# Kernel optimization log

Hardware: AMD Instinct MI355X
Metric: run time of the kernel (lower is better)

Reference implementation:

```python
import jax, jax.numpy as jnp
import numpy as np

N, K, B, D, T = 30000, 32, 8, 256, 10
NC = T + 1            # int_small_classes
LB_COL, UB_COL = 21, 22
INF = 1e18


def _ln(x, g, b, eps=1e-5):
    m = jnp.mean(x, axis=-1, keepdims=True)
    v = jnp.mean((x - m) ** 2, axis=-1, keepdims=True)
    return (x - m) * jax.lax.rsqrt(v + eps) * g + b


def _head(x, ng, nb, W1, b1, W2, b2, Wh, bh):
    # LayerNorm -> Linear -> GELU -> Linear -> GELU -> residual -> head (dropout off: eval)
    h = _ln(x, ng, nb)
    h = jax.nn.gelu(h @ W1.T + b1, approximate=False)
    h = jax.nn.gelu(h @ W2.T + b2, approximate=False)
    return (x + h) @ Wh.T + bh


def setup_inputs():
    key = jax.random.key(0)
    ks = jax.random.split(key, 32)
    s = 0.05
    inp = {}
    inp['evolved_tokens'] = jax.random.normal(ks[0], (B * K, D), jnp.float32)
    inp['var_batch'] = jnp.sort(jax.random.randint(ks[1], (N,), 0, B))
    aw = jax.random.uniform(ks[2], (N, K), jnp.float32)
    inp['attn_weights'] = aw / aw.sum(-1, keepdims=True)
    inp['var_types'] = jax.random.randint(ks[3], (N,), 0, 3)
    inp['z_var_0'] = jax.random.normal(ks[4], (N, D), jnp.float32)
    vf = 0.1 * jax.random.normal(ks[5], (N, 23), jnp.float32)
    lb = jnp.floor(jax.random.uniform(ks[6], (N,), minval=-5.0, maxval=0.0))
    ub = lb + jnp.floor(jax.random.uniform(ks[7], (N,), minval=0.0, maxval=30.0))
    ub = jnp.where(jax.random.uniform(ks[8], (N,)) < 0.1, 1e19, ub)
    inp['variable_features'] = vf.at[:, LB_COL].set(lb).at[:, UB_COL].set(ub)
    # deslice proj + fusion norm
    inp['Wp'] = s * jax.random.normal(ks[9], (D, D), jnp.float32)
    inp['bp'] = jnp.zeros((D,), jnp.float32)
    inp['fn_g'] = jnp.ones((D,), jnp.float32)
    inp['fn_b'] = jnp.zeros((D,), jnp.float32)
    # three decoder heads
    i = 10
    for name, out in (('bin', 1), ('ints', NC), ('intl', 1)):
        inp[name + '_ng'] = jnp.ones((D,), jnp.float32)
        inp[name + '_nb'] = jnp.zeros((D,), jnp.float32)
        inp[name + '_W1'] = s * jax.random.normal(ks[i], (D, D), jnp.float32)
        inp[name + '_b1'] = jnp.zeros((D,), jnp.float32)
        inp[name + '_W2'] = s * jax.random.normal(ks[i + 1], (D, D), jnp.float32)
        inp[name + '_b2'] = jnp.zeros((D,), jnp.float32)
        inp[name + '_Wh'] = s * jax.random.normal(ks[i + 2], (out, D), jnp.float32)
        inp[name + '_bh'] = (jnp.full((out,), -0.5, jnp.float32) if name == 'bin'
                             else jnp.zeros((out,), jnp.float32))
        i += 3
    return inp


def reference(evolved_tokens, var_batch, attn_weights, var_types, z_var_0,
              variable_features, Wp, bp, fn_g, fn_b,
              bin_ng, bin_nb, bin_W1, bin_b1, bin_W2, bin_b2, bin_Wh, bin_bh,
              ints_ng, ints_nb, ints_W1, ints_b1, ints_W2, ints_b2, ints_Wh, ints_bh,
              intl_ng, intl_nb, intl_W1, intl_b1, intl_W2, intl_b2, intl_Wh, intl_bh):
    # 1. deslice: attn_weights @ projected evolved tokens of the variable's graph
    proj = evolved_tokens @ Wp.T + bp          # [B*K, D]
    tok3 = proj.reshape(B, K, D)
    z_des = jnp.einsum('nk,nkd->nd', attn_weights, tok3[var_batch])  # [N, D]
    # 2. residual fusion + LayerNorm
    z_out = _ln(z_des + z_var_0, fn_g, fn_b)
    # 3. routing (extract_int_routing)
    lb = variable_features[:, LB_COL]
    ub = variable_features[:, UB_COL]
    is_int = var_types == 2
    finite = (jnp.abs(lb) < INF) & (jnp.abs(ub) < INF)
    mask_int_small = is_int & finite & ((ub - lb) <= T)
    mask_int_large = is_int & ~mask_int_small
    mask_bin = var_types == 1
    offsets = jnp.floor(lb)                                   # [N]
    ranges = jnp.clip(jnp.ceil(ub) - offsets + 1.0, 1.0, NC).astype(jnp.int32)  # [N]
    # 4. decode. Heads are evaluated densely on all N rows; the original's
    #    gather->MLP->scatter equals row-selection of these dense outputs.
    prob_bin = jax.nn.sigmoid(_head(z_out, bin_ng, bin_nb, bin_W1, bin_b1,
                                    bin_W2, bin_b2, bin_Wh, bin_bh))   # [N, 1]
    logits = _head(z_out, ints_ng, ints_nb, ints_W1, ints_b1,
                   ints_W2, ints_b2, ints_Wh, ints_bh)                 # [N, NC]
    valid = jnp.arange(NC)[None, :] < ranges[:, None]
    logits = jnp.where(valid, logits, -1e9)  # dynamic logit masking of invalid classes
    pred_large = _head(z_out, intl_ng, intl_nb, intl_W1, intl_b1,
                       intl_W2, intl_b2, intl_Wh, intl_bh)             # [N, 1]
    return (z_out, prob_bin, logits, pred_large,
            mask_bin, mask_int_small, mask_int_large, offsets, ranges)
```

## Files before the change

### kernel.cpp

```cpp
#include <hip/hip_runtime.h>
#include <math.h>

#define NV   30000
#define DD   256
#define KK   32
#define NCLS 11
#define NT   469

#define OZ  0
#define OPB 7680000
#define OLG 7710000
#define OPL 8040000
#define OMB 8070000
#define OMS 8100000
#define OML 8130000
#define OOF 8160000
#define ORG 8190000

typedef __bf16 bf16x8 __attribute__((ext_vector_type(8)));
typedef float  f32x4  __attribute__((ext_vector_type(4)));

__device__ __forceinline__ unsigned short f2b(float f) {
    unsigned u = __float_as_uint(f);
    u += 0x7fffu + ((u >> 16) & 1u);
    return (unsigned short)(u >> 16);
}

__device__ __forceinline__ float gelu_f(float x) {
    float x2 = x * x;
    float m = x * __builtin_fmaf(-0.0713548163f, x2, -1.5957691216f);
    float e = __expf(m);
    return x * __builtin_amdgcn_rcpf(1.0f + e);
}

__device__ __forceinline__ int swz(int row) { return (row + (row >> 3)) & 7; }
__device__ __forceinline__ int lidx(int row, int col) {
    return row * 256 + ((((col) >> 3) ^ swz(row)) << 3) + (col & 7);
}
__device__ __forceinline__ int physchunk(int ck, int row) {
    return (ck & ~7) | ((ck & 7) ^ swz(row));
}

struct WP {
    const float *W1, *ng, *nb, *b1, *W2, *Wh;
    unsigned short *W1e, *W2b, *Whb;
    float *b1e, *swh;
    int nc;
};

__global__ void k_prep(const float* __restrict__ et, const float* __restrict__ Wp,
                       const float* __restrict__ bp, unsigned short* __restrict__ projT,
                       const float* __restrict__ vf, const int* __restrict__ vt,
                       float* __restrict__ out,
                       WP wa, WP wb, WP wc) {
    __shared__ float es[DD];
    __shared__ float red[4], red2[4];
    if (blockIdx.y == 0) {
        int r = blockIdx.x, c = threadIdx.x;
        es[c] = et[r * DD + c];
        __syncthreads();
        const float4* w4 = (const float4*)(Wp + c * DD);
        float a0 = 0.f, a1 = 0.f, a2 = 0.f, a3 = 0.f;
#pragma unroll 16
        for (int d = 0; d < DD / 4; ++d) {
            float4 w = w4[d];
            a0 += es[4 * d] * w.x;
            a1 += es[4 * d + 1] * w.y;
            a2 += es[4 * d + 2] * w.z;
            a3 += es[4 * d + 3] * w.w;
        }
        float acc = bp[c] + ((a0 + a1) + (a2 + a3));
        projT[c * DD + r] = f2b(acc);
        return;
    }
    if (blockIdx.y == 4) {
        int n = blockIdx.x * 256 + threadIdx.x;
        if (n < NV) {
            float lb = vf[n * 23 + 21], ub = vf[n * 23 + 22];
            int t = vt[n];
            bool is_int = (t == 2);
            bool finite = (fabsf(lb) < 1e18f) && (fabsf(ub) < 1e18f);
            bool small_ = is_int && finite && (ub - lb <= 10.0f);
            float off = floorf(lb);
            float rngf = ceilf(ub) - off + 1.0f;
            rngf = fminf(fmaxf(rngf, 1.0f), (float)NCLS);
            out[OMB + n] = (t == 1) ? 1.0f : 0.0f;
            out[OMS + n] = small_ ? 1.0f : 0.0f;
            out[OML + n] = (is_int && !small_) ? 1.0f : 0.0f;
            out[OOF + n] = off;
            out[ORG + n] = (float)((int)rngf);
        }
        return;
    }
    WP wp = (blockIdx.y == 1) ? wa : ((blockIdx.y == 2) ? wb : wc);
    int j = blockIdx.x, d = threadIdx.x;
    float v1 = wp.W1[j * DD + d];
    wp.W1e[j * DD + d] = f2b(v1 * wp.ng[d]);
    wp.W2b[j * DD + d] = f2b(wp.W2[j * DD + d]);
    float p2 = 0.f;
    if (j < 16) {
        p2 = (j < wp.nc) ? wp.Wh[j * DD + d] : 0.f;
        wp.Whb[j * DD + d] = f2b(p2);
    }
    float p = v1 * wp.nb[d];
#pragma unroll
    for (int m = 1; m < 64; m <<= 1) { p += __shfl_xor(p, m); p2 += __shfl_xor(p2, m); }
    if ((d & 63) == 0) { red[d >> 6] = p; red2[d >> 6] = p2; }
    __syncthreads();
    if (d == 0) {
        wp.b1e[j] = wp.b1[j] + red[0] + red[1] + red[2] + red[3];
        if (j < 16) wp.swh[j] = red2[0] + red2[1] + red2[2] + red2[3];
    }
}

__global__ __launch_bounds__(512)
void k_zout(const unsigned short* __restrict__ projT, const int* __restrict__ vb,
            const float* __restrict__ aw, const float* __restrict__ z0,
            const float* __restrict__ g, const float* __restrict__ b,
            const unsigned short* __restrict__ Whb, const float* __restrict__ swh,
            float* __restrict__ out, unsigned short* __restrict__ zhat,
            float* __restrict__ zwhT) {
    __shared__ unsigned short Al[64 * 256];
    __shared__ float sqs[64 * 8], sqq[64 * 8];
    __shared__ float mvm[64], mvr[64], sig[64];
    __shared__ float gs[DD], bs[DD];
    __shared__ float swhs[48];
    int tid = threadIdx.x;
    int lane = tid & 63, wv = tid >> 6;
    int l15 = lane & 15, lq = lane >> 4;
    int n0 = blockIdx.x * 64;

    int bmin = vb[n0];
    int bmax = vb[(n0 + 63 < NV) ? (n0 + 63) : (NV - 1)];

    if (tid < 256) gs[tid] = g[tid];
    else           bs[tid - 256] = b[tid - 256];
    if (tid < 48) swhs[tid] = swh[tid];
    {
        uint4 z4 = make_uint4(0, 0, 0, 0);
        uint4* dst = (uint4*)Al;
#pragma unroll
        for (int j = 0; j < 4; ++j) dst[tid + j * 512] = z4;
    }
    __syncthreads();
    {
        int r = tid >> 3, sub = tid & 7;
        int n = n0 + r;
        if (n < NV) {
            int bb = vb[n];
            float4 a4 = *(const float4*)(aw + (size_t)n * KK + sub * 4);
            int j0 = bb * 32 + sub * 4;
            int phys = r * 256 + (physchunk(j0 >> 3, r) << 3) + (j0 & 7);
            ushort4 u;
            u.x = f2b(a4.x); u.y = f2b(a4.y); u.z = f2b(a4.z); u.w = f2b(a4.w);
            *(ushort4*)(Al + phys) = u;
        }
    }
    __syncthreads();

    int nb0 = wv * 32;
    f32x4 acc[4][2];
#pragma unroll
    for (int mt = 0; mt < 4; ++mt)
#pragma unroll
        for (int nt = 0; nt < 2; ++nt) acc[mt][nt] = f32x4{0.f, 0.f, 0.f, 0.f};

    {
        const unsigned short* Bb = projT + (size_t)(nb0 + l15) * DD + lq * 8;
        for (int ks = bmin; ks <= bmax; ++ks) {
            bf16x8 bfr[2];
#pragma unroll
            for (int nt = 0; nt < 2; ++nt)
                bfr[nt] = *(const bf16x8*)(Bb + nt * 16 * DD + ks * 32);
            int ck = ks * 4 + lq;
#pragma unroll
            for (int mt = 0; mt < 4; ++mt) {
                int row = mt * 16 + l15;
                bf16x8 afr = *(const bf16x8*)(Al + row * 256 + (physchunk(ck, row) << 3));
#pragma unroll
                for (int nt = 0; nt < 2; ++nt)
                    acc[mt][nt] = __builtin_amdgcn_mfma_f32_16x16x32_bf16(afr, bfr[nt], acc[mt][nt], 0, 0, 0);
            }
        }
    }
#pragma unroll
    for (int mt = 0; mt < 4; ++mt)
#pragma unroll
        for (int nt = 0; nt < 2; ++nt) {
            int col = nb0 + nt * 16 + l15;
#pragma unroll
            for (int r = 0; r < 4; ++r) {
                int n = n0 + mt * 16 + lq * 4 + r;
                float zv = (n < NV) ? z0[(size_t)n * DD + col] : 0.f;
                acc[mt][nt][r] += zv;
            }
        }
#pragma unroll
    for (int mt = 0; mt < 4; ++mt)
#pragma unroll
        for (int r = 0; r < 4; ++r) {
            float s = acc[mt][0][r] + acc[mt][1][r];
            float q = acc[mt][0][r] * acc[mt][0][r] + acc[mt][1][r] * acc[mt][1][r];
#pragma unroll
            for (int m = 1; m < 16; m <<= 1) { s += __shfl_xor(s, m); q += __shfl_xor(q, m); }
            if (l15 == 0) { int row = mt * 16 + lq * 4 + r; sqs[row * 8 + wv] = s; sqq[row * 8 + wv] = q; }
        }
    __syncthreads();
    if (tid < 64) {
        float s = 0.f, q = 0.f;
#pragma unroll
        for (int w = 0; w < 8; ++w) { s += sqs[tid * 8 + w]; q += sqq[tid * 8 + w]; }
        float mean = s * (1.f / DD);
        float var  = q * (1.f / DD) - mean * mean;
        mvm[tid] = mean; mvr[tid] = rsqrtf(var + 1e-5f);
    }
    __syncthreads();
    float zb[4][2][4];
#pragma unroll
    for (int mt = 0; mt < 4; ++mt)
#pragma unroll
        for (int nt = 0; nt < 2; ++nt) {
            int col = nb0 + nt * 16 + l15;
#pragma unroll
            for (int r = 0; r < 4; ++r) {
                int row = mt * 16 + lq * 4 + r;
                float z = (acc[mt][nt][r] - mvm[row]) * mvr[row] * gs[col] + bs[col];
                zb[mt][nt][r] = z;
                int n = n0 + row;
                if (n < NV) out[OZ + (size_t)n * DD + col] = z;
            }
        }
#pragma unroll
    for (int mt = 0; mt < 4; ++mt)
#pragma unroll
        for (int r = 0; r < 4; ++r) {
            float s = zb[mt][0][r] + zb[mt][1][r];
            float q = zb[mt][0][r] * zb[mt][0][r] + zb[mt][1][r] * zb[mt][1][r];
#pragma unroll
            for (int m = 1; m < 16; m <<= 1) { s += __shfl_xor(s, m); q += __shfl_xor(q, m); }
            if (l15 == 0) { int row = mt * 16 + lq * 4 + r; sqs[row * 8 + wv] = s; sqq[row * 8 + wv] = q; }
        }
    __syncthreads();
    if (tid < 64) {
        float s = 0.f, q = 0.f;
#pragma unroll
        for (int w = 0; w < 8; ++w) { s += sqs[tid * 8 + w]; q += sqq[tid * 8 + w]; }
        float m2 = s * (1.f / DD);
        float v2 = q * (1.f / DD) - m2 * m2;
        float r2 = rsqrtf(v2 + 1e-5f);
        mvm[tid] = m2; mvr[tid] = r2; sig[tid] = (v2 + 1e-5f) * r2;
    }
    __syncthreads();
#pragma unroll
    for (int mt = 0; mt < 4; ++mt)
#pragma unroll
        for (int nt = 0; nt < 2; ++nt) {
            int col = nb0 + nt * 16 + l15;
#pragma unroll
            for (int r = 0; r < 4; ++r) {
                int row = mt * 16 + lq * 4 + r;
                Al[lidx(row, col)] = f2b((zb[mt][nt][r] - mvm[row]) * mvr[row]);
            }
        }
    __syncthreads();
    if (wv < 4) {
        f32x4 ac2[3];
#pragma unroll
        for (int mf = 0; mf < 3; ++mf) ac2[mf] = f32x4{0.f, 0.f, 0.f, 0.f};
        const unsigned short* Ab = Whb + (size_t)l15 * DD + lq * 8;
        int rowb = wv * 16 + l15;
#pragma unroll
        for (int ks = 0; ks < 8; ++ks) {
            int ck = ks * 4 + lq;
            bf16x8 bb2 = *(const bf16x8*)(Al + rowb * 256 + (physchunk(ck, rowb) << 3));
#pragma unroll
            for (int mf = 0; mf < 3; ++mf) {
                bf16x8 aa2 = *(const bf16x8*)(Ab + (size_t)mf * 16 * DD + ks * 32);
                ac2[mf] = __builtin_amdgcn_mfma_f32_16x16x32_bf16(aa2, bb2, ac2[mf], 0, 0, 0);
            }
        }
        int nl = wv * 16 + l15;
        float sg = sig[nl], mu = mvm[nl];
#pragma unroll
        for (int mf = 0; mf < 3; ++mf)
#pragma unroll
            for (int r = 0; r < 4; ++r) {
                int o = mf * 16 + lq * 4 + r;
                zwhT[(size_t)blockIdx.x * 3072 + o * 64 + nl] = sg * ac2[mf][r] + mu * swhs[o];
            }
    }
    {
        uint4* dstg = (uint4*)(zhat + (size_t)n0 * 256);
        const uint4* srcl = (const uint4*)Al;
#pragma unroll
        for (int j = 0; j < 4; ++j) dstg[tid + j * 512] = srcl[tid + j * 512];
    }
}

struct HeadP {
    const unsigned short *W1e, *W2b, *Whb;
    const float *b1e, *b2, *bh;
    int nc;
};

__global__ __launch_bounds__(512, 4)
void k_heads(const unsigned short* __restrict__ zhat, const float* __restrict__ zwhT,
             const float* __restrict__ ranges,
             HeadP h0, HeadP h1p, HeadP h2p,
             float* __restrict__ opb, float* __restrict__ olg, float* __restrict__ opl) {
    __shared__ unsigned short hl1[64 * 256];
    __shared__ unsigned short hl2[64 * 256];
    __shared__ float b1s[DD], b2s[DD];
    __shared__ float zws[16 * 64];
    __shared__ float rgs[64];
    __shared__ float bhs[16];

    int head = blockIdx.x / NT;
    int tile = blockIdx.x % NT;
    HeadP hp = (head == 0) ? h0 : ((head == 1) ? h1p : h2p);
    int nc = hp.nc;
    int n0 = tile * 64;
    int tid = threadIdx.x, lane = tid & 63, wv = tid >> 6;
    int l15 = lane & 15, lq = lane >> 4;
    int M0 = wv * 32;

    {
        const uint4* src = (const uint4*)(zhat + (size_t)n0 * 256);
        uint4* dst = (uint4*)hl1;
#pragma unroll
        for (int j = 0; j < 4; ++j) dst[tid + j * 512] = src[tid + j * 512];
    }
    if (tid < 256) b1s[tid] = hp.b1e[tid];
    else           b2s[tid - 256] = hp.b2[tid - 256];
    ((float2*)zws)[tid] = ((const float2*)(zwhT + (size_t)(tile * 3 + head) * 1024))[tid];
    if (tid < 64) { int n = n0 + tid; rgs[tid] = (n < NV) ? ranges[n] : 0.f; }
    else if (tid < 80) { int o = tid - 64; bhs[o] = (o < nc) ? hp.bh[o] : 0.f; }
    __syncthreads();

    const unsigned short* Ab1 = hp.W1e + (size_t)(M0 + l15) * DD + lq * 8;
    const unsigned short* Ab2 = hp.W2b + (size_t)(M0 + l15) * DD + lq * 8;

    f32x4 acc[2][4];
#pragma unroll
    for (int mt = 0; mt < 2; ++mt)
#pragma unroll
        for (int nt = 0; nt < 4; ++nt) acc[mt][nt] = f32x4{0.f, 0.f, 0.f, 0.f};

    bf16x8 afr[3][2];
#pragma unroll
    for (int mt = 0; mt < 2; ++mt) {
        afr[0][mt] = *(const bf16x8*)(Ab1 + mt * 16 * DD);
        afr[1][mt] = *(const bf16x8*)(Ab1 + mt * 16 * DD + 32);
    }

#pragma unroll
    for (int ks = 0; ks < 8; ++ks) {
        int cur = ks % 3;
        if (ks < 6) {
#pragma unroll
            for (int mt = 0; mt < 2; ++mt)
                afr[(ks + 2) % 3][mt] = *(const bf16x8*)(Ab1 + mt * 16 * DD + (ks + 2) * 32);
        }
        int ck = ks * 4 + lq;
        bf16x8 bfr[4];
#pragma unroll
        for (int nt = 0; nt < 4; ++nt) {
            int row = nt * 16 + l15;
            bfr[nt] = *(const bf16x8*)(hl1 + row * 256 + (physchunk(ck, row) << 3));
        }
#pragma unroll
        for (int nt = 0; nt < 4; ++nt)
#pragma unroll
            for (int mt = 0; mt < 2; ++mt)
                acc[mt][nt] = __builtin_amdgcn_mfma_f32_16x16x32_bf16(afr[cur][mt], bfr[nt], acc[mt][nt], 0, 0, 0);
    }

#pragma unroll
    for (int mt = 0; mt < 2; ++mt) {
        afr[0][mt] = *(const bf16x8*)(Ab2 + mt * 16 * DD);
        afr[1][mt] = *(const bf16x8*)(Ab2 + mt * 16 * DD + 32);
    }

#pragma unroll
    for (int mt = 0; mt < 2; ++mt) {
        int jb = M0 + mt * 16 + lq * 4;
        float4 bias = *(const float4*)(b1s + jb);
        int chunk = jb >> 3;
#pragma unroll
        for (int nt = 0; nt < 4; ++nt) {
            int n = nt * 16 + l15;
            ushort4 u;
            u.x = f2b(gelu_f(acc[mt][nt][0] + bias.x));
            u.y = f2b(gelu_f(acc[mt][nt][1] + bias.y));
            u.z = f2b(gelu_f(acc[mt][nt][2] + bias.z));
            u.w = f2b(gelu_f(acc[mt][nt][3] + bias.w));
            *(ushort4*)(hl2 + n * 256 + (physchunk(chunk, n) << 3) + (jb & 7)) = u;
        }
    }
    __syncthreads();

#pragma unroll
    for (int mt = 0; mt < 2; ++mt)
#pragma unroll
        for (int nt = 0; nt < 4; ++nt) acc[mt][nt] = f32x4{0.f, 0.f, 0.f, 0.f};
#pragma unroll
    for (int ks = 0; ks < 8; ++ks) {
        int cur = ks % 3;
        if (ks < 6) {
#pragma unroll
            for (int mt = 0; mt < 2; ++mt)
                afr[(ks + 2) % 3][mt] = *(const bf16x8*)(Ab2 + mt * 16 * DD + (ks + 2) * 32);
        }
        int ck = ks * 4 + lq;
        bf16x8 bfr[4];
#pragma unroll
        for (int nt = 0; nt < 4; ++nt) {
            int row = nt * 16 + l15;
            bfr[nt] = *(const bf16x8*)(hl2 + row * 256 + (physchunk(ck, row) << 3));
        }
#pragma unroll
        for (int nt = 0; nt < 4; ++nt)
#pragma unroll
            for (int mt = 0; mt < 2; ++mt)
                acc[mt][nt] = __builtin_amdgcn_mfma_f32_16x16x32_bf16(afr[cur][mt], bfr[nt], acc[mt][nt], 0, 0, 0);
    }

    bf16x8 apr = *(const bf16x8*)(hp.Whb + (size_t)l15 * DD + wv * 32 + lq * 8);

#pragma unroll
    for (int mt = 0; mt < 2; ++mt) {
        int jb = M0 + mt * 16 + lq * 4;
        float4 bias = *(const float4*)(b2s + jb);
        int chunk = jb >> 3;
#pragma unroll
        for (int nt = 0; nt < 4; ++nt) {
            int n = nt * 16 + l15;
            ushort4 u;
            u.x = f2b(gelu_f(acc[mt][nt][0] + bias.x));
            u.y = f2b(gelu_f(acc[mt][nt][1] + bias.y));
            u.z = f2b(gelu_f(acc[mt][nt][2] + bias.z));
            u.w = f2b(gelu_f(acc[mt][nt][3] + bias.w));
            *(ushort4*)(hl1 + n * 256 + (physchunk(chunk, n) << 3) + (jb & 7)) = u;
        }
    }
    __syncthreads();

    f32x4 ap[4];
#pragma unroll
    for (int nt = 0; nt < 4; ++nt) ap[nt] = f32x4{0.f, 0.f, 0.f, 0.f};
    {
        int ck = wv * 4 + lq;
#pragma unroll
        for (int nt = 0; nt < 4; ++nt) {
            int row = nt * 16 + l15;
            bf16x8 bfr = *(const bf16x8*)(hl1 + row * 256 + (physchunk(ck, row) << 3));
            ap[nt] = __builtin_amdgcn_mfma_f32_16x16x32_bf16(apr, bfr, ap[nt], 0, 0, 0);
        }
    }
    {
        float* pb = (float*)hl2;
#pragma unroll
        for (int nt = 0; nt < 4; ++nt)
#pragma unroll
            for (int r = 0; r < 4; ++r)
                pb[wv * 1024 + (lq * 4 + r) * 64 + nt * 16 + l15] = ap[nt][r];
    }
    __syncthreads();

    const float* pb = (const float*)hl2;
    for (int idx = tid; idx < 64 * nc; idx += 512) {
        int o = idx >> 6, n = idx & 63;
        float val = bhs[o] + zws[o * 64 + n];
#pragma unroll
        for (int w = 0; w < 8; ++w) val += pb[w * 1024 + o * 64 + n];
        int ng = n0 + n;
        if (ng < NV) {
            if (head == 0)      opb[ng] = __builtin_amdgcn_rcpf(1.f + __expf(-val));
            else if (head == 2) opl[ng] = val;
            else {
                int rng = (int)rgs[n];
                olg[(size_t)ng * NCLS + o] = (o < rng) ? val : -1e9f;
            }
        }
    }
}

extern "C" void kernel_launch(void* const* d_in, const int* in_sizes, int n_in,
                              void* d_out, int out_size, void* d_ws, size_t ws_size,
                              hipStream_t stream) {
    const float* et = (const float*)d_in[0];
    const int*   vb = (const int*)d_in[1];
    const float* aw = (const float*)d_in[2];
    const int*   vt = (const int*)d_in[3];
    const float* z0 = (const float*)d_in[4];
    const float* vf = (const float*)d_in[5];
    const float* Wp = (const float*)d_in[6];
    const float* bp = (const float*)d_in[7];
    const float* fg = (const float*)d_in[8];
    const float* fb = (const float*)d_in[9];
    float* out = (float*)d_out;

    char* ws = (char*)d_ws;
    unsigned short* projT = (unsigned short*)ws;
    float* b1e           = (float*)(ws + 131072);
    unsigned short* W1e  = (unsigned short*)(ws + 134144);
    unsigned short* W2b  = (unsigned short*)(ws + 527360);
    unsigned short* Whb  = (unsigned short*)(ws + 920576);
    float* swh           = (float*)(ws + 945152);
    float* zwhT          = (float*)(ws + 945408);
    unsigned short* zhat = (unsigned short*)(ws + 6708480);

    WP wps[3];
    for (int h = 0; h < 3; ++h) {
        wps[h].W1 = (const float*)d_in[12 + 8 * h];
        wps[h].ng = (const float*)d_in[10 + 8 * h];
        wps[h].nb = (const float*)d_in[11 + 8 * h];
        wps[h].b1 = (const float*)d_in[13 + 8 * h];
        wps[h].W2 = (const float*)d_in[14 + 8 * h];
        wps[h].Wh = (const float*)d_in[16 + 8 * h];
        wps[h].W1e = W1e + h * 65536;
        wps[h].W2b = W2b + h * 65536;
        wps[h].Whb = Whb + h * 4096;
        wps[h].b1e = b1e + h * 256;
        wps[h].swh = swh + h * 16;
        wps[h].nc  = (h == 1) ? NCLS : 1;
    }
    k_prep<<<dim3(256, 5), 256, 0, stream>>>(et, Wp, bp, projT, vf, vt, out,
                                             wps[0], wps[1], wps[2]);

    k_zout<<<NT, 512, 0, stream>>>(projT, vb, aw, z0, fg, fb, Whb, swh,
                                   out, zhat, zwhT);

    HeadP hps[3];
    for (int h = 0; h < 3; ++h) {
        hps[h].W1e = W1e + h * 65536;
        hps[h].W2b = W2b + h * 65536;
        hps[h].Whb = Whb + h * 4096;
        hps[h].b1e = b1e + h * 256;
        hps[h].b2  = (const float*)d_in[15 + 8 * h];
        hps[h].bh  = (const float*)d_in[17 + 8 * h];
        hps[h].nc  = (h == 1) ? NCLS : 1;
    }
    k_heads<<<3 * NT, 512, 0, stream>>>(zhat, zwhT, out + ORG,
                                        hps[0], hps[1], hps[2],
                                        out + OPB, out + OLG, out + OPL);
}
```

Measured before the change: 235.6 us.

## Fuse z_out computation and three decoder heads into a single kernel

Merges the z_out/LayerNorm kernel with the per-head MLP kernel. Each 64-row block now keeps the normalized tile in LDS and loops over the three heads itself, so the bf16 zhat and zwhT round-trips through global memory go away, along with one launch. The final head projection is also reworked as a direct MFMA on four waves instead of an 8-way partial-sum reduction. In exchange, the grid drops from 3*NT blocks to NT blocks, and each block runs the three heads serially, which cuts parallelism across the GPU.

```diff
diff --git a/kernel.cpp b/kernel.cpp
--- a/kernel.cpp
+++ b/kernel.cpp
@@ -113,22 +113,37 @@
     }
 }
 
-__global__ __launch_bounds__(512)
-void k_zout(const unsigned short* __restrict__ projT, const int* __restrict__ vb,
+struct HeadP {
+    const unsigned short *W1e, *W2b, *Whb;
+    const float *b1e, *b2, *bh;
+    int nc;
+};
+
+__global__ __launch_bounds__(512, 4)
+void k_main(const unsigned short* __restrict__ projT, const int* __restrict__ vb,
             const float* __restrict__ aw, const float* __restrict__ z0,
             const float* __restrict__ g, const float* __restrict__ b,
             const unsigned short* __restrict__ Whb, const float* __restrict__ swh,
-            float* __restrict__ out, unsigned short* __restrict__ zhat,
-            float* __restrict__ zwhT) {
+            const float* __restrict__ ranges,
+            HeadP h0, HeadP h1p, HeadP h2p,
+            float* __restrict__ out, float* __restrict__ opb,
+            float* __restrict__ olg, float* __restrict__ opl) {
     __shared__ unsigned short Al[64 * 256];
-    __shared__ float sqs[64 * 8], sqq[64 * 8];
+    __shared__ unsigned short hl2[64 * 256];
+    __shared__ float b1s[DD], b2s[DD];
+    __shared__ float zws[48 * 64];
     __shared__ float mvm[64], mvr[64], sig[64];
-    __shared__ float gs[DD], bs[DD];
     __shared__ float swhs[48];
+
     int tid = threadIdx.x;
     int lane = tid & 63, wv = tid >> 6;
     int l15 = lane & 15, lq = lane >> 4;
     int n0 = blockIdx.x * 64;
+
+    float* gs = zws;
+    float* bs = zws + 256;
+    float* sqs = (float*)hl2;
+    float* sqq = (float*)hl2 + 512;
 
     int bmin = vb[n0];
     int bmax = vb[(n0 + 63 < NV) ? (n0 + 63) : (NV - 1)];
@@ -164,7 +179,6 @@
     for (int mt = 0; mt < 4; ++mt)
 #pragma unroll
         for (int nt = 0; nt < 2; ++nt) acc[mt][nt] = f32x4{0.f, 0.f, 0.f, 0.f};
-
     {
         const unsigned short* Bb = projT + (size_t)(nb0 + l15) * DD + lq * 8;
         for (int ks = bmin; ks <= bmax; ++ks) {
@@ -215,7 +229,6 @@
         mvm[tid] = mean; mvr[tid] = rsqrtf(var + 1e-5f);
     }
     __syncthreads();
-    float zb[4][2][4];
 #pragma unroll
     for (int mt = 0; mt < 4; ++mt)
 #pragma unroll
@@ -225,7 +238,7 @@
             for (int r = 0; r < 4; ++r) {
                 int row = mt * 16 + lq * 4 + r;
                 float z = (acc[mt][nt][r] - mvm[row]) * mvr[row] * gs[col] + bs[col];
-                zb[mt][nt][r] = z;
+                acc[mt][nt][r] = z;
                 int n = n0 + row;
                 if (n < NV) out[OZ + (size_t)n * DD + col] = z;
             }
@@ -234,8 +247,8 @@
     for (int mt = 0; mt < 4; ++mt)
 #pragma unroll
         for (int r = 0; r < 4; ++r) {
-            float s = zb[mt][0][r] + zb[mt][1][r];
-            float q = zb[mt][0][r] * zb[mt][0][r] + zb[mt][1][r] * zb[mt][1][r];
+            float s = acc[mt][0][r] + acc[mt][1][r];
+            float q = acc[mt][0][r] * acc[mt][0][r] + acc[mt][1][r] * acc[mt][1][r];
 #pragma unroll
             for (int m = 1; m < 16; m <<= 1) { s += __shfl_xor(s, m); q += __shfl_xor(q, m); }
             if (l15 == 0) { int row = mt * 16 + lq * 4 + r; sqs[row * 8 + wv] = s; sqq[row * 8 + wv] = q; }
@@ -259,7 +272,7 @@
 #pragma unroll
             for (int r = 0; r < 4; ++r) {
                 int row = mt * 16 + lq * 4 + r;
-                Al[lidx(row, col)] = f2b((zb[mt][nt][r] - mvm[row]) * mvr[row]);
+                Al[lidx(row, col)] = f2b((acc[mt][nt][r] - mvm[row]) * mvr[row]);
             }
         }
     __syncthreads();
@@ -286,200 +299,152 @@
 #pragma unroll
             for (int r = 0; r < 4; ++r) {
                 int o = mf * 16 + lq * 4 + r;
-                zwhT[(size_t)blockIdx.x * 3072 + o * 64 + nl] = sg * ac2[mf][r] + mu * swhs[o];
-            }
-    }
-    {
-        uint4* dstg = (uint4*)(zhat + (size_t)n0 * 256);
-        const uint4* srcl = (const uint4*)Al;
-#pragma unroll
-        for (int j = 0; j < 4; ++j) dstg[tid + j * 512] = srcl[tid + j * 512];
-    }
-}
-
-struct HeadP {
-    const unsigned short *W1e, *W2b, *Whb;
-    const float *b1e, *b2, *bh;
-    int nc;
-};
-
-__global__ __launch_bounds__(512, 4)
-void k_heads(const unsigned short* __restrict__ zhat, const float* __restrict__ zwhT,
-             const float* __restrict__ ranges,
-             HeadP h0, HeadP h1p, HeadP h2p,
-             float* __restrict__ opb, float* __restrict__ olg, float* __restrict__ opl) {
-    __shared__ unsigned short hl1[64 * 256];
-    __shared__ unsigned short hl2[64 * 256];
-    __shared__ float b1s[DD], b2s[DD];
-    __shared__ float zws[16 * 64];
-    __shared__ float rgs[64];
-    __shared__ float bhs[16];
-
-    int head = blockIdx.x / NT;
-    int tile = blockIdx.x % NT;
-    HeadP hp = (head == 0) ? h0 : ((head == 1) ? h1p : h2p);
-    int nc = hp.nc;
-    int n0 = tile * 64;
-    int tid = threadIdx.x, lane = tid & 63, wv = tid >> 6;
-    int l15 = lane & 15, lq = lane >> 4;
-    int M0 = wv * 32;
-
-    {
-        const uint4* src = (const uint4*)(zhat + (size_t)n0 * 256);
-        uint4* dst = (uint4*)hl1;
-#pragma unroll
-        for (int j = 0; j < 4; ++j) dst[tid + j * 512] = src[tid + j * 512];
-    }
-    if (tid < 256) b1s[tid] = hp.b1e[tid];
-    else           b2s[tid - 256] = hp.b2[tid - 256];
-    ((float2*)zws)[tid] = ((const float2*)(zwhT + (size_t)(tile * 3 + head) * 1024))[tid];
-    if (tid < 64) { int n = n0 + tid; rgs[tid] = (n < NV) ? ranges[n] : 0.f; }
-    else if (tid < 80) { int o = tid - 64; bhs[o] = (o < nc) ? hp.bh[o] : 0.f; }
-    __syncthreads();
-
-    const unsigned short* Ab1 = hp.W1e + (size_t)(M0 + l15) * DD + lq * 8;
-    const unsigned short* Ab2 = hp.W2b + (size_t)(M0 + l15) * DD + lq * 8;
-
-    f32x4 acc[2][4];
-#pragma unroll
-    for (int mt = 0; mt < 2; ++mt)
-#pragma unroll
-        for (int nt = 0; nt < 4; ++nt) acc[mt][nt] = f32x4{0.f, 0.f, 0.f, 0.f};
-
-    bf16x8 afr[3][2];
-#pragma unroll
-    for (int mt = 0; mt < 2; ++mt) {
-        afr[0][mt] = *(const bf16x8*)(Ab1 + mt * 16 * DD);
-        afr[1][mt] = *(const bf16x8*)(Ab1 + mt * 16 * DD + 32);
-    }
-
-#pragma unroll
-    for (int ks = 0; ks < 8; ++ks) {
-        int cur = ks % 3;
-        if (ks < 6) {
-#pragma unroll
-            for (int mt = 0; mt < 2; ++mt)
-                afr[(ks + 2) % 3][mt] = *(const bf16x8*)(Ab1 + mt * 16 * DD + (ks + 2) * 32);
-        }
-        int ck = ks * 4 + lq;
-        bf16x8 bfr[4];
-#pragma unroll
-        for (int nt = 0; nt < 4; ++nt) {
-            int row = nt * 16 + l15;
-            bfr[nt] = *(const bf16x8*)(hl1 + row * 256 + (physchunk(ck, row) << 3));
-        }
-#pragma unroll
-        for (int nt = 0; nt < 4; ++nt)
-#pragma unroll
-            for (int mt = 0; mt < 2; ++mt)
-                acc[mt][nt] = __builtin_amdgcn_mfma_f32_16x16x32_bf16(afr[cur][mt], bfr[nt], acc[mt][nt], 0, 0, 0);
-    }
-
-#pragma unroll
-    for (int mt = 0; mt < 2; ++mt) {
-        afr[0][mt] = *(const bf16x8*)(Ab2 + mt * 16 * DD);
-        afr[1][mt] = *(const bf16x8*)(Ab2 + mt * 16 * DD + 32);
-    }
-
-#pragma unroll
-    for (int mt = 0; mt < 2; ++mt) {
-        int jb = M0 + mt * 16 + lq * 4;
-        float4 bias = *(const float4*)(b1s + jb);
-        int chunk = jb >> 3;
-#pragma unroll
-        for (int nt = 0; nt < 4; ++nt) {
-            int n = nt * 16 + l15;
-            ushort4 u;
-            u.x = f2b(gelu_f(acc[mt][nt][0] + bias.x));
-            u.y = f2b(gelu_f(acc[mt][nt][1] + bias.y));
-            u.z = f2b(gelu_f(acc[mt][nt][2] + bias.z));
-            u.w = f2b(gelu_f(acc[mt][nt][3] + bias.w));
-            *(ushort4*)(hl2 + n * 256 + (physchunk(chunk, n) << 3) + (jb & 7)) = u;
-        }
-    }
-    __syncthreads();
-
-#pragma unroll
-    for (int mt = 0; mt < 2; ++mt)
-#pragma unroll
-        for (int nt = 0; nt < 4; ++nt) acc[mt][nt] = f32x4{0.f, 0.f, 0.f, 0.f};
-#pragma unroll
-    for (int ks = 0; ks < 8; ++ks) {
-        int cur = ks % 3;
-        if (ks < 6) {
-#pragma unroll
-            for (int mt = 0; mt < 2; ++mt)
-                afr[(ks + 2) % 3][mt] = *(const bf16x8*)(Ab2 + mt * 16 * DD + (ks + 2) * 32);
-        }
-        int ck = ks * 4 + lq;
-        bf16x8 bfr[4];
-#pragma unroll
-        for (int nt = 0; nt < 4; ++nt) {
-            int row = nt * 16 + l15;
-            bfr[nt] = *(const bf16x8*)(hl2 + row * 256 + (physchunk(ck, row) << 3));
-        }
-#pragma unroll
-        for (int nt = 0; nt < 4; ++nt)
-#pragma unroll
-            for (int mt = 0; mt < 2; ++mt)
-                acc[mt][nt] = __builtin_amdgcn_mfma_f32_16x16x32_bf16(afr[cur][mt], bfr[nt], acc[mt][nt], 0, 0, 0);
-    }
-
-    bf16x8 apr = *(const bf16x8*)(hp.Whb + (size_t)l15 * DD + wv * 32 + lq * 8);
-
-#pragma unroll
-    for (int mt = 0; mt < 2; ++mt) {
-        int jb = M0 + mt * 16 + lq * 4;
-        float4 bias = *(const float4*)(b2s + jb);
-        int chunk = jb >> 3;
-#pragma unroll
-        for (int nt = 0; nt < 4; ++nt) {
-            int n = nt * 16 + l15;
-            ushort4 u;
-            u.x = f2b(gelu_f(acc[mt][nt][0] + bias.x));
-            u.y = f2b(gelu_f(acc[mt][nt][1] + bias.y));
-            u.z = f2b(gelu_f(acc[mt][nt][2] + bias.z));
-            u.w = f2b(gelu_f(acc[mt][nt][3] + bias.w));
-            *(ushort4*)(hl1 + n * 256 + (physchunk(chunk, n) << 3) + (jb & 7)) = u;
-        }
-    }
-    __syncthreads();
-
-    f32x4 ap[4];
-#pragma unroll
-    for (int nt = 0; nt < 4; ++nt) ap[nt] = f32x4{0.f, 0.f, 0.f, 0.f};
-    {
-        int ck = wv * 4 + lq;
-#pragma unroll
-        for (int nt = 0; nt < 4; ++nt) {
-            int row = nt * 16 + l15;
-            bf16x8 bfr = *(const bf16x8*)(hl1 + row * 256 + (physchunk(ck, row) << 3));
-            ap[nt] = __builtin_amdgcn_mfma_f32_16x16x32_bf16(apr, bfr, ap[nt], 0, 0, 0);
-        }
-    }
-    {
-        float* pb = (float*)hl2;
-#pragma unroll
-        for (int nt = 0; nt < 4; ++nt)
-#pragma unroll
-            for (int r = 0; r < 4; ++r)
-                pb[wv * 1024 + (lq * 4 + r) * 64 + nt * 16 + l15] = ap[nt][r];
-    }
-    __syncthreads();
-
-    const float* pb = (const float*)hl2;
-    for (int idx = tid; idx < 64 * nc; idx += 512) {
-        int o = idx >> 6, n = idx & 63;
-        float val = bhs[o] + zws[o * 64 + n];
-#pragma unroll
-        for (int w = 0; w < 8; ++w) val += pb[w * 1024 + o * 64 + n];
-        int ng = n0 + n;
-        if (ng < NV) {
-            if (head == 0)      opb[ng] = __builtin_amdgcn_rcpf(1.f + __expf(-val));
-            else if (head == 2) opl[ng] = val;
-            else {
-                int rng = (int)rgs[n];
-                olg[(size_t)ng * NCLS + o] = (o < rng) ? val : -1e9f;
+                zws[o * 64 + nl] = sg * ac2[mf][r] + mu * swhs[o];
+            }
+    }
+    __syncthreads();
+
+    for (int head = 0; head < 3; ++head) {
+        HeadP hp = (head == 0) ? h0 : ((head == 1) ? h1p : h2p);
+        if (tid < 256) b1s[tid] = hp.b1e[tid];
+        else           b2s[tid - 256] = hp.b2[tid - 256];
+
+        const unsigned short* Ab1 = hp.W1e + (size_t)((wv * 32) + l15) * DD + lq * 8;
+        const unsigned short* Ab2 = hp.W2b + (size_t)((wv * 32) + l15) * DD + lq * 8;
+        int M0 = wv * 32;
+
+        f32x4 hacc[2][4];
+#pragma unroll
+        for (int mt = 0; mt < 2; ++mt)
+#pragma unroll
+            for (int nt = 0; nt < 4; ++nt) hacc[mt][nt] = f32x4{0.f, 0.f, 0.f, 0.f};
+
+        bf16x8 afr[3][2];
+#pragma unroll
+        for (int mt = 0; mt < 2; ++mt) {
+            afr[0][mt] = *(const bf16x8*)(Ab1 + mt * 16 * DD);
+            afr[1][mt] = *(const bf16x8*)(Ab1 + mt * 16 * DD + 32);
+        }
+        __syncthreads();
+
+#pragma unroll
+        for (int ks = 0; ks < 8; ++ks) {
+            int cur = ks % 3;
+            if (ks < 6) {
+#pragma unroll
+                for (int mt = 0; mt < 2; ++mt)
+                    afr[(ks + 2) % 3][mt] = *(const bf16x8*)(Ab1 + mt * 16 * DD + (ks + 2) * 32);
+            }
+            int ck = ks * 4 + lq;
+            bf16x8 bfr[4];
+#pragma unroll
+            for (int nt = 0; nt < 4; ++nt) {
+                int row = nt * 16 + l15;
+                bfr[nt] = *(const bf16x8*)(Al + row * 256 + (physchunk(ck, row) << 3));
+            }
+#pragma unroll
+            for (int nt = 0; nt < 4; ++nt)
+#pragma unroll
+                for (int mt = 0; mt < 2; ++mt)
+                    hacc[mt][nt] = __builtin_amdgcn_mfma_f32_16x16x32_bf16(afr[cur][mt], bfr[nt], hacc[mt][nt], 0, 0, 0);
+        }
+#pragma unroll
+        for (int mt = 0; mt < 2; ++mt) {
+            afr[0][mt] = *(const bf16x8*)(Ab2 + mt * 16 * DD);
+            afr[1][mt] = *(const bf16x8*)(Ab2 + mt * 16 * DD + 32);
+        }
+#pragma unroll
+        for (int mt = 0; mt < 2; ++mt) {
+            int jb = M0 + mt * 16 + lq * 4;
+            float4 bias = *(const float4*)(b1s + jb);
+            int chunk = jb >> 3;
+#pragma unroll
+            for (int nt = 0; nt < 4; ++nt) {
+                int n = nt * 16 + l15;
+                ushort4 u;
+                u.x = f2b(gelu_f(hacc[mt][nt][0] + bias.x));
+                u.y = f2b(gelu_f(hacc[mt][nt][1] + bias.y));
+                u.z = f2b(gelu_f(hacc[mt][nt][2] + bias.z));
+                u.w = f2b(gelu_f(hacc[mt][nt][3] + bias.w));
+                *(ushort4*)(hl2 + n * 256 + (physchunk(chunk, n) << 3) + (jb & 7)) = u;
+            }
+        }
+        __syncthreads();
+
+#pragma unroll
+        for (int mt = 0; mt < 2; ++mt)
+#pragma unroll
+            for (int nt = 0; nt < 4; ++nt) hacc[mt][nt] = f32x4{0.f, 0.f, 0.f, 0.f};
+#pragma unroll
+        for (int ks = 0; ks < 8; ++ks) {
+            int cur = ks % 3;
+            if (ks < 6) {
+#pragma unroll
+                for (int mt = 0; mt < 2; ++mt)
+                    afr[(ks + 2) % 3][mt] = *(const bf16x8*)(Ab2 + mt * 16 * DD + (ks + 2) * 32);
+            }
+            int ck = ks * 4 + lq;
+            bf16x8 bfr[4];
+#pragma unroll
+            for (int nt = 0; nt < 4; ++nt) {
+                int row = nt * 16 + l15;
+                bfr[nt] = *(const bf16x8*)(hl2 + row * 256 + (physchunk(ck, row) << 3));
+            }
+#pragma unroll
+            for (int nt = 0; nt < 4; ++nt)
+#pragma unroll
+                for (int mt = 0; mt < 2; ++mt)
+                    hacc[mt][nt] = __builtin_amdgcn_mfma_f32_16x16x32_bf16(afr[cur][mt], bfr[nt], hacc[mt][nt], 0, 0, 0);
+        }
+        __syncthreads();
+
+#pragma unroll
+        for (int mt = 0; mt < 2; ++mt) {
+            int jb = M0 + mt * 16 + lq * 4;
+            float4 bias = *(const float4*)(b2s + jb);
+            int chunk = jb >> 3;
+#pragma unroll
+            for (int nt = 0; nt < 4; ++nt) {
+                int n = nt * 16 + l15;
+                ushort4 u;
+                u.x = f2b(gelu_f(hacc[mt][nt][0] + bias.x));
+                u.y = f2b(gelu_f(hacc[mt][nt][1] + bias.y));
+                u.z = f2b(gelu_f(hacc[mt][nt][2] + bias.z));
+                u.w = f2b(gelu_f(hacc[mt][nt][3] + bias.w));
+                *(ushort4*)(hl2 + n * 256 + (physchunk(chunk, n) << 3) + (jb & 7)) = u;
+            }
+        }
+        __syncthreads();
+
+        if (wv < 4) {
+            f32x4 pc = f32x4{0.f, 0.f, 0.f, 0.f};
+            const unsigned short* Ah = hp.Whb + (size_t)l15 * DD + lq * 8;
+            int tokr = wv * 16 + l15;
+#pragma unroll
+            for (int ks = 0; ks < 8; ++ks) {
+                int ck = ks * 4 + lq;
+                bf16x8 bb2 = *(const bf16x8*)(hl2 + tokr * 256 + (physchunk(ck, tokr) << 3));
+                bf16x8 aa2 = *(const bf16x8*)(Ah + ks * 32);
+                pc = __builtin_amdgcn_mfma_f32_16x16x32_bf16(aa2, bb2, pc, 0, 0, 0);
+            }
+            int tok = wv * 16 + l15;
+            int ng = n0 + tok;
+            if (ng < NV) {
+                if (head == 1) {
+                    int rng = (int)ranges[ng];
+#pragma unroll
+                    for (int r = 0; r < 4; ++r) {
+                        int o = lq * 4 + r;
+                        if (o < NCLS) {
+                            float val = pc[r] + hp.bh[o] + zws[o * 64 + tok];
+                            olg[(size_t)ng * NCLS + o] = (o < rng) ? val : -1e9f;
+                        }
+                    }
+                } else if (lq == 0) {
+                    float val = pc[0] + hp.bh[0] + zws[tok];
+                    if (head == 0) opb[ng] = __builtin_amdgcn_rcpf(1.f + __expf(-val));
+                    else           opl[ng] = val;
+                }
             }
         }
     }
@@ -507,8 +472,6 @@
     unsigned short* W2b  = (unsigned short*)(ws + 527360);
     unsigned short* Whb  = (unsigned short*)(ws + 920576);
     float* swh           = (float*)(ws + 945152);
-    float* zwhT          = (float*)(ws + 945408);
-    unsigned short* zhat = (unsigned short*)(ws + 6708480);
 
     WP wps[3];
     for (int h = 0; h < 3; ++h) {
@@ -528,9 +491,6 @@
     k_prep<<<dim3(256, 5), 256, 0, stream>>>(et, Wp, bp, projT, vf, vt, out,
                                              wps[0], wps[1], wps[2]);
 
-    k_zout<<<NT, 512, 0, stream>>>(projT, vb, aw, z0, fg, fb, Whb, swh,
-                                   out, zhat, zwhT);
-
     HeadP hps[3];
     for (int h = 0; h < 3; ++h) {
         hps[h].W1e = W1e + h * 65536;
@@ -541,7 +501,7 @@
         hps[h].bh  = (const float*)d_in[17 + 8 * h];
         hps[h].nc  = (h == 1) ? NCLS : 1;
     }
-    k_heads<<<3 * NT, 512, 0, stream>>>(zhat, zwhT, out + ORG,
-                                        hps[0], hps[1], hps[2],
-                                        out + OPB, out + OLG, out + OPL);
-}
+    k_main<<<NT, 512, 0, stream>>>(projT, vb, aw, z0, fg, fb, Whb, swh,
+                                   out + ORG, hps[0], hps[1], hps[2],
+                                   out, out + OPB, out + OLG, out + OPL);
+}
```

Result: slower. 241.8 us (+2.6%).
